# Kernel tuning notes

Measured on AMD Instinct MI355X. Metric: run time of the kernel, lower is better.

Reference implementation:

```python
import jax, jax.numpy as jnp
import numpy as np
from jax import lax


def _sobel_kernels():
    # separable construction: smooth=[1,2,1], deriv=[-1,0,1]
    s = jnp.array([1.0, 2.0, 1.0], dtype=jnp.float32)
    d = jnp.array([-1.0, 0.0, 1.0], dtype=jnp.float32)
    kx = jnp.einsum('i,j,k->ijk', s, s, d)  # gradient along W
    ky = jnp.einsum('i,j,k->ijk', s, d, s)  # gradient along H
    kz = jnp.einsum('i,j,k->ijk', d, s, s)  # gradient along D
    return jnp.stack([kx, ky, kz])[:, None]  # [3, 1, 3, 3, 3] OIDHW


def setup_inputs() -> dict:
    key = jax.random.key(0)
    image = jax.random.normal(key, (4, 1, 128, 256, 256), dtype=jnp.float32)
    return {"image": image}


def reference(image):
    k = _sobel_kernels()
    # one conv producing Gx, Gy, Gz as 3 output channels (same math as 3 conv3d calls)
    G = lax.conv_general_dilated(
        image, k,
        window_strides=(1, 1, 1),
        padding=[(1, 1), (1, 1), (1, 1)],
        dimension_numbers=('NCDHW', 'OIDHW', 'NCDHW'),
    )  # [B, 3, D, H, W]
    mag = jnp.sqrt(jnp.sum(G * G, axis=1, keepdims=True) + 1e-8)  # [B,1,D,H,W]
    return jnp.concatenate([image, mag], axis=1)  # [B,2,D,H,W]
```

## Files before the change

### kernel.cpp

```cpp
#include <hip/hip_runtime.h>
#include <math.h>

namespace {
constexpr int B  = 4;
constexpr int D  = 128;
constexpr int H  = 256;
constexpr int W  = 256;
constexpr int TH = 16;
constexpr int TW = 64;
constexpr int CH = 32;
constexpr int AS = 68;
typedef float nf4 __attribute__((ext_vector_type(4)));
}

#define SMOOTH3(o, p0, p1, p2) \
  o.x = fmaf(2.f, p1.x, p0.x + p2.x); \
  o.y = fmaf(2.f, p1.y, p0.y + p2.y); \
  o.z = fmaf(2.f, p1.z, p0.z + p2.z); \
  o.w = fmaf(2.f, p1.w, p0.w + p2.w);
#define DIFF3(o, p0, p2) \
  o.x = p2.x - p0.x; o.y = p2.y - p0.y; o.z = p2.z - p0.z; o.w = p2.w - p0.w;

__device__ __forceinline__ void st_nt(float* p, float4 v) {
  nf4 nv; nv.x = v.x; nv.y = v.y; nv.z = v.z; nv.w = v.w;
  __builtin_nontemporal_store(nv, (nf4*)p);
}

__global__ __launch_bounds__(256, 4)
void sobel_fused(const float* __restrict__ img, float* __restrict__ out) {
  __shared__ float sa[2][18 * AS];
  __shared__ float sb[2][18 * AS];

  const int t  = threadIdx.x;
  const int r  = t >> 4;
  const int cg = (t & 15) << 2;
  const int w0 = blockIdx.x * TW;
  const int h0 = blockIdx.y * TH;
  const int bz = blockIdx.z;
  const int batch = bz >> 2;
  const int d0    = (bz & 3) * CH;

  const float* imgB = img + (size_t)batch * ((size_t)D * H * W);
  float* out0 = out + (size_t)batch * ((size_t)2 * D * H * W);
  float* out1 = out0 + (size_t)D * H * W;

  const int  gh0    = h0 + r - 1;
  const int  gh1    = h0 + r + 15;
  const bool row0In = ((unsigned)gh0 < (unsigned)H);
  const bool pass1  = (r < 2);
  const bool row1In = pass1 && ((unsigned)gh1 < (unsigned)H);
  const bool hasM   = (w0 + cg) > 0;
  const bool hasP   = (w0 + cg + 4) < W;

  const float4 z4 = {0.f, 0.f, 0.f, 0.f};
  float4 U0 = z4, U1 = z4, U2 = z4;
  float4 V0 = z4, V1 = z4, V2 = z4;
  float4 T0 = z4, T1 = z4, T2 = z4;

  float4 px0 = z4, px1 = z4;
  float  pm0 = 0.f, pp0 = 0.f, pm1 = 0.f, pp1 = 0.f;

#define ISSUE(jj) do {                                                     \
    const int p_ = d0 + (jj) - 1;                                          \
    const bool pin_ = (p_ >= 0) && (p_ < D);                               \
    px0 = z4; pm0 = 0.f; pp0 = 0.f;                                        \
    px1 = z4; pm1 = 0.f; pp1 = 0.f;                                        \
    if (pin_ && row0In) {                                                  \
      const float* rp = imgB + ((size_t)p_ * H + gh0) * W + (w0 + cg);     \
      px0 = *(const float4*)rp;                                            \
      if (hasM) pm0 = rp[-1];                                              \
      if (hasP) pp0 = rp[4];                                               \
    }                                                                      \
    if (pin_ && row1In) {                                                  \
      const float* rp = imgB + ((size_t)p_ * H + gh1) * W + (w0 + cg);     \
      px1 = *(const float4*)rp;                                            \
      if (hasM) pm1 = rp[-1];                                              \
      if (hasP) pp1 = rp[4];                                               \
    }                                                                      \
  } while (0)

  ISSUE(0);

  for (int j = 0; j <= CH + 1; ++j) {
    const int p   = d0 + j - 1;
    const bool cpin = (p >= 0) && (p < D);
    const bool wr0  = (j >= 1) && (j <= CH);
    const int buf = j & 1;

    {
      float4 av, bv;
      av.x = fmaf(2.f, px0.x, pm0   + px0.y);
      av.y = fmaf(2.f, px0.y, px0.x + px0.z);
      av.z = fmaf(2.f, px0.z, px0.y + px0.w);
      av.w = fmaf(2.f, px0.w, px0.z + pp0);
      bv.x = px0.y - pm0; bv.y = px0.z - px0.x;
      bv.z = px0.w - px0.y; bv.w = pp0 - px0.z;
      *(float4*)&sa[buf][r * AS + cg] = av;
      *(float4*)&sb[buf][r * AS + cg] = bv;
      if (wr0 && cpin && row0In && r >= 1)
        st_nt(&out0[((size_t)p * H + gh0) * W + (w0 + cg)], px0);
    }
    if (pass1) {
      float4 av, bv;
      av.x = fmaf(2.f, px1.x, pm1   + px1.y);
      av.y = fmaf(2.f, px1.y, px1.x + px1.z);
      av.z = fmaf(2.f, px1.z, px1.y + px1.w);
      av.w = fmaf(2.f, px1.w, px1.z + pp1);
      bv.x = px1.y - pm1; bv.y = px1.z - px1.x;
      bv.z = px1.w - px1.y; bv.w = pp1 - px1.z;
      *(float4*)&sa[buf][(r + 16) * AS + cg] = av;
      *(float4*)&sb[buf][(r + 16) * AS + cg] = bv;
      if (wr0 && cpin && r == 0)
        st_nt(&out0[((size_t)p * H + gh1) * W + (w0 + cg)], px1);
    }

    if (j <= CH) ISSUE(j + 1);

    __syncthreads();

    float4 a0 = *(const float4*)&sa[buf][(r    ) * AS + cg];
    float4 a1 = *(const float4*)&sa[buf][(r + 1) * AS + cg];
    float4 a2 = *(const float4*)&sa[buf][(r + 2) * AS + cg];
    float4 b0 = *(const float4*)&sb[buf][(r    ) * AS + cg];
    float4 b1 = *(const float4*)&sb[buf][(r + 1) * AS + cg];
    float4 b2 = *(const float4*)&sb[buf][(r + 2) * AS + cg];
    float4 Un, Vn, Tn;
    SMOOTH3(Un, a0, a1, a2);
    DIFF3(Tn, a0, a2);
    SMOOTH3(Vn, b0, b1, b2);
    U0 = U1; U1 = U2; U2 = Un;
    V0 = V1; V1 = V2; V2 = Vn;
    T0 = T1; T1 = T2; T2 = Tn;

    if (j >= 2) {
      const int dout = d0 + j - 2;
      float4 gx, gy, gz, m;
      SMOOTH3(gx, V0, V1, V2);
      SMOOTH3(gy, T0, T1, T2);
      DIFF3(gz, U0, U2);
      m.x = sqrtf(fmaf(gx.x, gx.x, fmaf(gy.x, gy.x, fmaf(gz.x, gz.x, 1e-8f))));
      m.y = sqrtf(fmaf(gx.y, gx.y, fmaf(gy.y, gy.y, fmaf(gz.y, gz.y, 1e-8f))));
      m.z = sqrtf(fmaf(gx.z, gx.z, fmaf(gy.z, gy.z, fmaf(gz.z, gz.z, 1e-8f))));
      m.w = sqrtf(fmaf(gx.w, gx.w, fmaf(gy.w, gy.w, fmaf(gz.w, gz.w, 1e-8f))));
      st_nt(&out1[((size_t)dout * H + (h0 + r)) * W + (w0 + cg)], m);
    }
  }
#undef ISSUE
}

extern "C" void kernel_launch(void* const* d_in, const int* in_sizes, int n_in,
                              void* d_out, int out_size, void* d_ws, size_t ws_size,
                              hipStream_t stream) {
  const float* img = (const float*)d_in[0];
  float* out = (float*)d_out;
  dim3 grid(W / TW, H / TH, B * (D / CH));
  sobel_fused<<<grid, dim3(256), 0, stream>>>(img, out);
}
```

Measured before the change: 377.4 us.

## Replace shared-memory H-halo exchange with direct global loads of neighbor rows

```diff
diff --git a/kernel.cpp b/kernel.cpp
--- a/kernel.cpp
+++ b/kernel.cpp
@@ -9,7 +9,6 @@
 constexpr int TH = 16;
 constexpr int TW = 64;
 constexpr int CH = 32;
-constexpr int AS = 68;
 typedef float nf4 __attribute__((ext_vector_type(4)));
 }
 
@@ -20,6 +19,13 @@
   o.w = fmaf(2.f, p1.w, p0.w + p2.w);
 #define DIFF3(o, p0, p2) \
   o.x = p2.x - p0.x; o.y = p2.y - p0.y; o.z = p2.z - p0.z; o.w = p2.w - p0.w;
+#define WPASS(av, bv, xv, xm, xp) \
+  av.x = fmaf(2.f, xv.x, (xm) + xv.y); \
+  av.y = fmaf(2.f, xv.y, xv.x + xv.z); \
+  av.z = fmaf(2.f, xv.z, xv.y + xv.w); \
+  av.w = fmaf(2.f, xv.w, xv.z + (xp)); \
+  bv.x = xv.y - (xm); bv.y = xv.z - xv.x; \
+  bv.z = xv.w - xv.y;  bv.w = (xp) - xv.z;
 
 __device__ __forceinline__ void st_nt(float* p, float4 v) {
   nf4 nv; nv.x = v.x; nv.y = v.y; nv.z = v.z; nv.w = v.w;
@@ -28,9 +34,6 @@
 
 __global__ __launch_bounds__(256, 4)
 void sobel_fused(const float* __restrict__ img, float* __restrict__ out) {
-  __shared__ float sa[2][18 * AS];
-  __shared__ float sb[2][18 * AS];
-
   const int t  = threadIdx.x;
   const int r  = t >> 4;
   const int cg = (t & 15) << 2;
@@ -44,93 +47,68 @@
   float* out0 = out + (size_t)batch * ((size_t)2 * D * H * W);
   float* out1 = out0 + (size_t)D * H * W;
 
-  const int  gh0    = h0 + r - 1;
-  const int  gh1    = h0 + r + 15;
-  const bool row0In = ((unsigned)gh0 < (unsigned)H);
-  const bool pass1  = (r < 2);
-  const bool row1In = pass1 && ((unsigned)gh1 < (unsigned)H);
-  const bool hasM   = (w0 + cg) > 0;
-  const bool hasP   = (w0 + cg + 4) < W;
+  const int  gh   = h0 + r;
+  const bool hasM = (w0 + cg) > 0;
+  const bool hasP = (w0 + cg + 4) < W;
+  const bool rowM = gh > 0;
+  const bool rowP = (gh + 1) < H;
 
   const float4 z4 = {0.f, 0.f, 0.f, 0.f};
   float4 U0 = z4, U1 = z4, U2 = z4;
   float4 V0 = z4, V1 = z4, V2 = z4;
   float4 T0 = z4, T1 = z4, T2 = z4;
 
-  float4 px0 = z4, px1 = z4;
-  float  pm0 = 0.f, pp0 = 0.f, pm1 = 0.f, pp1 = 0.f;
+  float4 x0 = z4, x1 = z4, x2 = z4;
+  float  m0 = 0.f, m1 = 0.f, m2 = 0.f;
+  float  p0 = 0.f, p1 = 0.f, p2 = 0.f;
 
-#define ISSUE(jj) do {                                                     \
-    const int p_ = d0 + (jj) - 1;                                          \
-    const bool pin_ = (p_ >= 0) && (p_ < D);                               \
-    px0 = z4; pm0 = 0.f; pp0 = 0.f;                                        \
-    px1 = z4; pm1 = 0.f; pp1 = 0.f;                                        \
-    if (pin_ && row0In) {                                                  \
-      const float* rp = imgB + ((size_t)p_ * H + gh0) * W + (w0 + cg);     \
-      px0 = *(const float4*)rp;                                            \
-      if (hasM) pm0 = rp[-1];                                              \
-      if (hasP) pp0 = rp[4];                                               \
-    }                                                                      \
-    if (pin_ && row1In) {                                                  \
-      const float* rp = imgB + ((size_t)p_ * H + gh1) * W + (w0 + cg);     \
-      px1 = *(const float4*)rp;                                            \
-      if (hasM) pm1 = rp[-1];                                              \
-      if (hasP) pp1 = rp[4];                                               \
-    }                                                                      \
+#define ISSUE(jj) do {                                                      \
+    const int p_ = d0 + (jj) - 1;                                           \
+    x0 = z4; x1 = z4; x2 = z4;                                              \
+    m0 = 0.f; m1 = 0.f; m2 = 0.f; p0 = 0.f; p1 = 0.f; p2 = 0.f;             \
+    if ((unsigned)p_ < (unsigned)D) {                                       \
+      const float* rp = imgB + ((size_t)p_ * H + gh) * W + (w0 + cg);       \
+      x1 = *(const float4*)rp;                                              \
+      if (hasM) m1 = rp[-1];                                                \
+      if (hasP) p1 = rp[4];                                                 \
+      if (rowM) {                                                           \
+        const float* q = rp - W;                                            \
+        x0 = *(const float4*)q;                                             \
+        if (hasM) m0 = q[-1];                                               \
+        if (hasP) p0 = q[4];                                                \
+      }                                                                     \
+      if (rowP) {                                                           \
+        const float* q = rp + W;                                            \
+        x2 = *(const float4*)q;                                             \
+        if (hasM) m2 = q[-1];                                               \
+        if (hasP) p2 = q[4];                                                \
+      }                                                                     \
+    }                                                                       \
   } while (0)
 
   ISSUE(0);
 
   for (int j = 0; j <= CH + 1; ++j) {
     const int p   = d0 + j - 1;
-    const bool cpin = (p >= 0) && (p < D);
-    const bool wr0  = (j >= 1) && (j <= CH);
-    const int buf = j & 1;
+    const bool wr0 = (j >= 1) && (j <= CH);
 
-    {
-      float4 av, bv;
-      av.x = fmaf(2.f, px0.x, pm0   + px0.y);
-      av.y = fmaf(2.f, px0.y, px0.x + px0.z);
-      av.z = fmaf(2.f, px0.z, px0.y + px0.w);
-      av.w = fmaf(2.f, px0.w, px0.z + pp0);
-      bv.x = px0.y - pm0; bv.y = px0.z - px0.x;
-      bv.z = px0.w - px0.y; bv.w = pp0 - px0.z;
-      *(float4*)&sa[buf][r * AS + cg] = av;
-      *(float4*)&sb[buf][r * AS + cg] = bv;
-      if (wr0 && cpin && row0In && r >= 1)
-        st_nt(&out0[((size_t)p * H + gh0) * W + (w0 + cg)], px0);
-    }
-    if (pass1) {
-      float4 av, bv;
-      av.x = fmaf(2.f, px1.x, pm1   + px1.y);
-      av.y = fmaf(2.f, px1.y, px1.x + px1.z);
-      av.z = fmaf(2.f, px1.z, px1.y + px1.w);
-      av.w = fmaf(2.f, px1.w, px1.z + pp1);
-      bv.x = px1.y - pm1; bv.y = px1.z - px1.x;
-      bv.z = px1.w - px1.y; bv.w = pp1 - px1.z;
-      *(float4*)&sa[buf][(r + 16) * AS + cg] = av;
-      *(float4*)&sb[buf][(r + 16) * AS + cg] = bv;
-      if (wr0 && cpin && r == 0)
-        st_nt(&out0[((size_t)p * H + gh1) * W + (w0 + cg)], px1);
-    }
+    float4 A0, B0, A1, B1, A2, B2;
+    WPASS(A0, B0, x0, m0, p0);
+    WPASS(A1, B1, x1, m1, p1);
+    WPASS(A2, B2, x2, m2, p2);
 
-    if (j <= CH) ISSUE(j + 1);
+    if (wr0)
+      st_nt(&out0[((size_t)p * H + gh) * W + (w0 + cg)], x1);
 
-    __syncthreads();
-
-    float4 a0 = *(const float4*)&sa[buf][(r    ) * AS + cg];
-    float4 a1 = *(const float4*)&sa[buf][(r + 1) * AS + cg];
-    float4 a2 = *(const float4*)&sa[buf][(r + 2) * AS + cg];
-    float4 b0 = *(const float4*)&sb[buf][(r    ) * AS + cg];
-    float4 b1 = *(const float4*)&sb[buf][(r + 1) * AS + cg];
-    float4 b2 = *(const float4*)&sb[buf][(r + 2) * AS + cg];
     float4 Un, Vn, Tn;
-    SMOOTH3(Un, a0, a1, a2);
-    DIFF3(Tn, a0, a2);
-    SMOOTH3(Vn, b0, b1, b2);
+    SMOOTH3(Un, A0, A1, A2);
+    DIFF3(Tn, A0, A2);
+    SMOOTH3(Vn, B0, B1, B2);
     U0 = U1; U1 = U2; U2 = Un;
     V0 = V1; V1 = V2; V2 = Vn;
     T0 = T1; T1 = T2; T2 = Tn;
+
+    if (j <= CH) ISSUE(j + 1);
 
     if (j >= 2) {
       const int dout = d0 + j - 2;
```

After: 405.1 us. +7.3%, slower.
